# Kernel optimization log

Hardware: AMD Instinct MI355X
Metric: run time of the kernel (lower is better)

## Reference

```python
import jax, jax.numpy as jnp
import numpy as np

L, C, H = 4, 512, 8
HD = C // H

def silu(x):
    return x * jax.nn.sigmoid(x)

def layernorm(x, g, b, eps=1e-5):
    m = x.mean(-1, keepdims=True)
    v = ((x - m) ** 2).mean(-1, keepdims=True)
    return (x - m) * jax.lax.rsqrt(v + eps) * g + b

def adaln(x, t, w, b):
    # x: (N,B,C), t: (B,C), w: (2C,C), b: (2C,)
    mod = silu(t) @ w.T + b
    scale, shift = jnp.split(mod, 2, axis=-1)
    return x * (1.0 + scale[None]) + shift[None]

def embed_rotary(x, pos):
    # x: (B,N,C), pos: (B,N,C,2) with [...,0]=cos, [...,1]=sin
    cos, sin = pos[..., 0], pos[..., 1]
    x2 = jnp.stack([-x[..., 1::2], x[..., 0::2]], axis=-1).reshape(x.shape)
    return x * cos + x2 * sin

def setup_inputs() -> dict:
    key = jax.random.key(0)
    ks = jax.random.split(key, 24)
    Nq, Nkv, B = 1024, 2048, 4
    query = jax.random.normal(ks[0], (Nq, B, C), jnp.float32)
    value = jax.random.normal(ks[1], (Nkv, B, C), jnp.float32)
    diff_ts = jax.random.normal(ks[2], (B, C), jnp.float32)
    # valid rotary codes: cos/sin of random angles
    aq = jax.random.uniform(ks[3], (B, Nq, C), jnp.float32, 0.0, 2 * np.pi)
    ak = jax.random.uniform(ks[4], (B, Nkv, C), jnp.float32, 0.0, 2 * np.pi)
    query_pos = jnp.stack([jnp.cos(aq), jnp.sin(aq)], axis=-1)
    value_pos = jnp.stack([jnp.cos(ak), jnp.sin(ak)], axis=-1)
    s = 0.02
    inp = dict(query=query, value=value, diff_ts=diff_ts,
               query_pos=query_pos, value_pos=value_pos,
               aw_attn=jax.random.normal(ks[5], (L, 2 * C, C)) * s,
               ab_attn=jax.random.normal(ks[6], (L, 2 * C)) * s,
               in_w=jax.random.normal(ks[7], (L, 3 * C, C)) * s,
               in_b=jnp.zeros((L, 3 * C)),
               out_w=jax.random.normal(ks[8], (L, C, C)) * s,
               out_b=jnp.zeros((L, C)),
               ln1_g=jnp.ones((L, C)), ln1_b=jnp.zeros((L, C)),
               aw_ffn=jax.random.normal(ks[9], (L, 2 * C, C)) * s,
               ab_ffn=jax.random.normal(ks[10], (L, 2 * C)) * s,
               w1=jax.random.normal(ks[11], (L, C, C)) * s,
               b1=jnp.zeros((L, C)),
               w2=jax.random.normal(ks[12], (L, C, C)) * s,
               b2=jnp.zeros((L, C)),
               ln2_g=jnp.ones((L, C)), ln2_b=jnp.zeros((L, C)))
    return inp

def _forward(query, value, diff_ts, query_pos, value_pos,
             aw_attn, ab_attn, in_w, in_b, out_w, out_b, ln1_g, ln1_b,
             aw_ffn, ab_ffn, w1, b1, w2, b2, ln2_g, ln2_b):
    Nq, B, _ = query.shape
    Nkv = value.shape[0]
    scaling = HD ** -0.5
    outputs = []
    q = query
    for i in range(L):
        # --- cross-attention layer ---
        aq = adaln(q, diff_ts, aw_attn[i], ab_attn[i])
        wq, wk, wv = jnp.split(in_w[i], 3, axis=0)
        bq, bk, bv = jnp.split(in_b[i], 3, axis=0)
        qp = (aq @ wq.T + bq) * scaling          # (Nq,B,C)
        kp = value @ wk.T + bk                    # (Nkv,B,C)
        vp = value @ wv.T + bv
        qb = embed_rotary(qp.transpose(1, 0, 2), query_pos)  # (B,Nq,C)
        kb = embed_rotary(kp.transpose(1, 0, 2), value_pos)  # (B,Nkv,C)
        vb = vp.transpose(1, 0, 2)
        qh = qb.reshape(B, Nq, H, HD).transpose(0, 2, 1, 3)   # (B,H,Nq,HD)
        kh = kb.reshape(B, Nkv, H, HD).transpose(0, 2, 1, 3)
        vh = vb.reshape(B, Nkv, H, HD).transpose(0, 2, 1, 3)
        scores = jnp.einsum('bhqd,bhkd->bhqk', qh, kh)
        attn = jax.nn.softmax(scores, axis=-1)
        o = jnp.einsum('bhqk,bhkd->bhqd', attn, vh)
        o = o.transpose(0, 2, 1, 3).reshape(B, Nq, C).transpose(1, 0, 2)  # (Nq,B,C)
        o = o @ out_w[i].T + out_b[i]
        q = layernorm(q + o, ln1_g[i], ln1_b[i])
        # --- feedforward layer (residual uses AdaLN-modulated x) ---
        xa = adaln(q, diff_ts, aw_ffn[i], ab_ffn[i])
        h = jax.nn.relu(xa @ w1[i].T + b1[i])
        h = h @ w2[i].T + b2[i]
        q = layernorm(xa + h, ln2_g[i], ln2_b[i])
        outputs.append(q)
    return jnp.stack(outputs)  # (L, Nq, B, C)

def reference(query, value, diff_ts, query_pos, value_pos,
              aw_attn, ab_attn, in_w, in_b, out_w, out_b, ln1_g, ln1_b,
              aw_ffn, ab_ffn, w1, b1, w2, b2, ln2_g, ln2_b):
    return _forward(query, value, diff_ts, query_pos, value_pos,
                    aw_attn, ab_attn, in_w, in_b, out_w, out_b, ln1_g, ln1_b,
                    aw_ffn, ab_ffn, w1, b1, w2, b2, ln2_g, ln2_b)
```

## Files before the change

kernel.cpp:

```cpp
#include <hip/hip_runtime.h>
#include <hip/hip_bf16.h>

typedef __hip_bfloat16 bf16;
typedef __attribute__((ext_vector_type(8))) short short8;
typedef __attribute__((ext_vector_type(4))) short s16x4;
typedef __attribute__((ext_vector_type(4))) float f32x4;

#define CDIM 512
#define BDIM 4
#define HDIM 8
#define HDQ  64
#define NQ   1024
#define NKV  2048
#define LAYERS 4
#define SPLIT 2

#if defined(__has_builtin)
#if __has_builtin(__builtin_amdgcn_global_load_lds)
#define USE_GLL 1
#endif
#endif

static __device__ __forceinline__ short f2s(float f) {
    bf16 h = __float2bfloat16(f);
    return *reinterpret_cast<short*>(&h);
}


__global__ __launch_bounds__(256) void convall_k(
    const float* __restrict__ s0, const float* __restrict__ s1,
    const float* __restrict__ s2, const float* __restrict__ s3,
    const float* __restrict__ s4,
    bf16* __restrict__ d0, bf16* __restrict__ d1, bf16* __restrict__ d2,
    bf16* __restrict__ d3, bf16* __restrict__ d4) {
    int gid = blockIdx.x * 256 + threadIdx.x;
    const float* src; bf16* dst; int off;
    if (gid < 1048576)      { src = s0; dst = d0; off = gid; }
    else if (gid < 1835008) { src = s1; dst = d1; off = gid - 1048576; }
    else if (gid < 2097152) { src = s2; dst = d2; off = gid - 1835008; }
    else if (gid < 2359296) { src = s3; dst = d3; off = gid - 2097152; }
    else                    { src = s4; dst = d4; off = gid - 2359296; }
    f32x4 v = *(const f32x4*)(src + (size_t)off * 4);
    s16x4 o;
    o[0] = f2s(v[0]); o[1] = f2s(v[1]); o[2] = f2s(v[2]); o[3] = f2s(v[3]);
    *(s16x4*)(dst + (size_t)off * 4) = o;
}

__global__ __launch_bounds__(256) void modall_k(const float* __restrict__ diff_ts,
    const float* __restrict__ aw_attn, const float* __restrict__ ab_attn,
    const float* __restrict__ aw_ffn,  const float* __restrict__ ab_ffn,
    float* __restrict__ mod) {
    int wv = blockIdx.x * 4 + (threadIdx.x >> 6);
    int lane = threadIdx.x & 63;
    int col  = wv & 1023;
    int b    = (wv >> 10) & 3;
    int kind = (wv >> 12) & 1;
    int l    = wv >> 13;
    const float* w = (kind ? aw_ffn : aw_attn) + ((size_t)l * 1024 + col) * CDIM + lane * 8;
    const float* tb = diff_ts + b * CDIM + lane * 8;
    f32x4 w0 = *(const f32x4*)w;
    f32x4 w1 = *(const f32x4*)(w + 4);
    f32x4 t0 = *(const f32x4*)tb;
    f32x4 t1 = *(const f32x4*)(tb + 4);
    #pragma unroll
    for (int j = 0; j < 4; ++j) {
        t0[j] = t0[j] / (1.f + __expf(-t0[j]));
        t1[j] = t1[j] / (1.f + __expf(-t1[j]));
    }
    f32x4 pp = w0 * t0 + w1 * t1;
    float acc = (pp[0] + pp[1]) + (pp[2] + pp[3]);
    #pragma unroll
    for (int off = 32; off; off >>= 1) acc += __shfl_xor(acc, off);
    if (lane == 0)
        mod[wv] = acc + (kind ? ab_ffn : ab_attn)[l * 1024 + col];
}

__global__ __launch_bounds__(256) void adaln_k(const float* __restrict__ x,
                                               const float* __restrict__ mod,
                                               bf16* __restrict__ outb) {
    int i = blockIdx.x * 256 + threadIdx.x;
    int c = i & 511;
    int b = (i >> 9) & 3;
    outb[i] = __float2bfloat16(x[i] * (1.f + mod[b * 1024 + c]) + mod[b * 1024 + 512 + c]);
}

__global__ __launch_bounds__(256) void ln_ad_k(const float* __restrict__ x,
                                               const float* __restrict__ res,
                                               const float* __restrict__ g,
                                               const float* __restrict__ bb,
                                               const float* __restrict__ mod,
                                               float* __restrict__ ln_f,
                                               float* __restrict__ ln_f2,
                                               float* __restrict__ ad_f,
                                               bf16* __restrict__ ad_b) {
    int row = blockIdx.x;
    int t = threadIdx.x;
    size_t base = (size_t)row * CDIM;
    float v0 = x[base + t] + res[base + t];
    float v1 = x[base + t + 256] + res[base + t + 256];
    float s1 = v0 + v1;
    float s2 = v0 * v0 + v1 * v1;
    #pragma unroll
    for (int off = 32; off; off >>= 1) {
        s1 += __shfl_xor(s1, off);
        s2 += __shfl_xor(s2, off);
    }
    __shared__ float a1[4], a2[4];
    int w = t >> 6;
    if ((t & 63) == 0) { a1[w] = s1; a2[w] = s2; }
    __syncthreads();
    s1 = a1[0] + a1[1] + a1[2] + a1[3];
    s2 = a2[0] + a2[1] + a2[2] + a2[3];
    float mean = s1 * (1.f / 512.f);
    float var = s2 * (1.f / 512.f) - mean * mean;
    float rs = rsqrtf(var + 1e-5f);
    float y0 = (v0 - mean) * rs * g[t] + bb[t];
    float y1 = (v1 - mean) * rs * g[t + 256] + bb[t + 256];
    if (ln_f)  { ln_f[base + t] = y0;  ln_f[base + t + 256] = y1; }
    if (ln_f2) { ln_f2[base + t] = y0; ln_f2[base + t + 256] = y1; }
    if (mod) {
        int b = row & 3;
        float o0 = y0 * (1.f + mod[b * 1024 + t]) + mod[b * 1024 + 512 + t];
        float o1 = y1 * (1.f + mod[b * 1024 + t + 256]) + mod[b * 1024 + 512 + t + 256];
        if (ad_f) { ad_f[base + t] = o0; ad_f[base + t + 256] = o1; }
        ad_b[base + t] = __float2bfloat16(o0);
        ad_b[base + t + 256] = __float2bfloat16(o1);
    }
}

template <int EPI, int WM, int NT, bool SWZ>
__global__ __launch_bounds__(256) void mgemm_k(
    const bf16* __restrict__ A, const bf16* __restrict__ Wt,
    const float* __restrict__ bias, void* __restrict__ out0v,
    int M, int N, int K,
    const float* __restrict__ pos, float scl, int Nseq) {
    __shared__ bf16 As[2][2][64 * 32];
    __shared__ bf16 Bs[2][2][64 * 32];
    int t = threadIdx.x;
    int w = t >> 6;
    int lane = t & 63;
    int l16 = lane & 15;
    int quad = lane >> 4;
    int wy = w >> 1, wx = w & 1;

    int bxi, byi;
    if (SWZ) {
        int nx = gridDim.x, ny = gridDim.y;
        int flat = blockIdx.y * nx + blockIdx.x;
        int nwg = nx * ny;
        int s = (flat & 7) * (nwg >> 3) + (flat >> 3);
        bxi = s % nx; byi = s / nx;
    } else {
        bxi = blockIdx.x; byi = blockIdx.y;
    }
    int bm = byi * 64;
    int bn = bxi * 64;

    int lr2 = lane >> 2;
    int lc4 = (lane & 3) ^ ((lane >> 3) & 3);

    f32x4 acc[WM][NT] = {};

    auto stage = [&](int buf, int k0) {
#if USE_GLL
        const bf16* sa = A + (size_t)(bm + w * 16 + lr2) * K + k0 + lc4 * 8;
        const bf16* sb = Wt + (size_t)(bn + w * 16 + lr2) * K + k0 + lc4 * 8;
        #pragma unroll
        for (int j = 0; j < 2; ++j) {
            __builtin_amdgcn_global_load_lds(
                (const unsigned int __attribute__((address_space(1)))*)(sa + j * 32),
                (unsigned int __attribute__((address_space(3)))*)(&As[buf][j][w * 512]),
                16, 0, 0);
            __builtin_amdgcn_global_load_lds(
                (const unsigned int __attribute__((address_space(1)))*)(sb + j * 32),
                (unsigned int __attribute__((address_space(3)))*)(&Bs[buf][j][w * 512]),
                16, 0, 0);
        }
#else
        for (int e = t; e < 512; e += 256) {
            int sub = e >> 8, c = e & 255;
            int row = c >> 2, c4 = c & 3;
            int srcc = c4 ^ ((row >> 1) & 3);
            *(uint4*)&As[buf][sub][row * 32 + c4 * 8] =
                *(const uint4*)(A + (size_t)(bm + row) * K + k0 + sub * 32 + srcc * 8);
            *(uint4*)&Bs[buf][sub][row * 32 + c4 * 8] =
                *(const uint4*)(Wt + (size_t)(bn + row) * K + k0 + sub * 32 + srcc * 8);
        }
#endif
    };

    stage(0, 0);
    int cur = 0;
    int rchunk = (quad ^ ((l16 >> 1) & 3)) * 8;

    for (int k0 = 0; k0 < K; k0 += 64) {
        bool more = (k0 + 64 < K);
        if (more) stage(cur ^ 1, k0 + 64);
#if USE_GLL
        if (more) asm volatile("s_waitcnt vmcnt(4)" ::: "memory");
        else      asm volatile("s_waitcnt vmcnt(0)" ::: "memory");
        __builtin_amdgcn_s_barrier();
#else
        __syncthreads();
#endif

        #pragma unroll
        for (int kk = 0; kk < 2; ++kk) {
            short8 af[WM], bfr[NT];
            #pragma unroll
            for (int mt = 0; mt < WM; ++mt)
                af[mt] = *(const short8*)
                    &As[cur][kk][((wy * WM + mt) * 16 + l16) * 32 + rchunk];
            #pragma unroll
            for (int nt = 0; nt < NT; ++nt)
                bfr[nt] = *(const short8*)
                    &Bs[cur][kk][((wx * NT + nt) * 16 + l16) * 32 + rchunk];
            #pragma unroll
            for (int mt = 0; mt < WM; ++mt)
                #pragma unroll
                for (int nt = 0; nt < NT; ++nt)
                    acc[mt][nt] = __builtin_amdgcn_mfma_f32_16x16x32_bf16(
                        af[mt], bfr[nt], acc[mt][nt], 0, 0, 0);
        }

#if USE_GLL
        __builtin_amdgcn_s_barrier();
#else
        __syncthreads();
#endif
        cur ^= 1;
    }

    #pragma unroll
    for (int nt = 0; nt < NT; ++nt) {
        int n = bn + (wx * NT + nt) * 16 + l16;
        float bnv = bias[n];
        #pragma unroll
        for (int mt = 0; mt < WM; ++mt) {
            #pragma unroll
            for (int r = 0; r < 4; ++r) {
                int m = bm + (wy * WM + mt) * 16 + quad * 4 + r;
                float v = acc[mt][nt][r] + bnv;
                if (EPI == 0) {
                    ((float*)out0v)[(size_t)m * N + n] = v;
                } else if (EPI == 1) {
                    ((bf16*)out0v)[(size_t)m * N + n] = __float2bfloat16(fmaxf(v, 0.f));
                } else {
                    v *= scl;
                    int c = n;
                    int nseq = m >> 2, b = m & 3;
                    float part = __shfl_xor(v, 1);
                    const float* pp = pos + (((size_t)b * Nseq + nseq) * CDIM + c) * 2;
                    float cs = pp[0], sn = pp[1];
                    float o = (l16 & 1) ? (v * cs + part * sn) : (v * cs - part * sn);
                    bf16* op = (bf16*)out0v +
                               ((size_t)(b * HDIM + (c >> 6)) * Nseq + nseq) * HDQ + (c & 63);
                    *op = __float2bfloat16(o);
                }
            }
        }
    }
}

__global__ __launch_bounds__(512) void kv8_k(
    const bf16* __restrict__ val, const bf16* __restrict__ Wk,
    const bf16* __restrict__ Wv, const float* __restrict__ biask,
    const float* __restrict__ biasv, bf16* __restrict__ kh,
    bf16* __restrict__ vt, const float* __restrict__ vpos) {
    __shared__ bf16 As[2][2][128 * 32];
    __shared__ bf16 Bk[2][2][64 * 32];
    __shared__ bf16 Bv[2][2][64 * 32];
    int t = threadIdx.x;
    int w = t >> 6;
    int lane = t & 63;
    int l16 = lane & 15;
    int quad = lane >> 4;
    int wy = w >> 1, wx = w & 1;

    int flat = blockIdx.x;
    int s = (flat & 7) * 64 + (flat >> 3);
    int bn = (s & 7) * 64;
    int bm = (s >> 3) * 128;
    const int K = CDIM;

    int lr2 = lane >> 2;
    int lc4 = (lane & 3) ^ ((lane >> 3) & 3);

    f32x4 acck[2][2] = {};
    f32x4 accv[2][2] = {};

    auto stage = [&](int buf, int k0) {
#if USE_GLL
        const bf16* sa = val + (size_t)(bm + w * 16 + lr2) * K + k0 + lc4 * 8;
        #pragma unroll
        for (int j = 0; j < 2; ++j) {
            __builtin_amdgcn_global_load_lds(
                (const unsigned int __attribute__((address_space(1)))*)(sa + j * 32),
                (unsigned int __attribute__((address_space(3)))*)(&As[buf][j][w * 512]),
                16, 0, 0);
        }
        if (w < 4) {
            const bf16* sk = Wk + (size_t)(bn + w * 16 + lr2) * K + k0 + lc4 * 8;
            #pragma unroll
            for (int j = 0; j < 2; ++j) {
                __builtin_amdgcn_global_load_lds(
                    (const unsigned int __attribute__((address_space(1)))*)(sk + j * 32),
                    (unsigned int __attribute__((address_space(3)))*)(&Bk[buf][j][w * 512]),
                    16, 0, 0);
            }
        } else {
            const bf16* sv = Wv + (size_t)(bn + (w - 4) * 16 + lr2) * K + k0 + lc4 * 8;
            #pragma unroll
            for (int j = 0; j < 2; ++j) {
                __builtin_amdgcn_global_load_lds(
                    (const unsigned int __attribute__((address_space(1)))*)(sv + j * 32),
                    (unsigned int __attribute__((address_space(3)))*)(&Bv[buf][j][(w - 4) * 512]),
                    16, 0, 0);
            }
        }
#else
        for (int u = t; u < 1024; u += 512) {
            int sub = u >> 9, c = u & 511;
            int row = c >> 2, c4 = c & 3;
            int srcc = c4 ^ ((row >> 1) & 3);
            *(uint4*)&As[buf][sub][row * 32 + c4 * 8] =
                *(const uint4*)(val + (size_t)(bm + row) * K + k0 + sub * 32 + srcc * 8);
        }
        {
            int u = t;
            int sub = u >> 8, c = u & 255;
            int row = c >> 2, c4 = c & 3;
            int srcc = c4 ^ ((row >> 1) & 3);
            *(uint4*)&Bk[buf][sub][row * 32 + c4 * 8] =
                *(const uint4*)(Wk + (size_t)(bn + row) * K + k0 + sub * 32 + srcc * 8);
            *(uint4*)&Bv[buf][sub][row * 32 + c4 * 8] =
                *(const uint4*)(Wv + (size_t)(bn + row) * K + k0 + sub * 32 + srcc * 8);
        }
#endif
    };

    stage(0, 0);
    int cur = 0;
    int rchunk = (quad ^ ((l16 >> 1) & 3)) * 8;

    for (int k0 = 0; k0 < K; k0 += 64) {
        bool more = (k0 + 64 < K);
        if (more) stage(cur ^ 1, k0 + 64);
#if USE_GLL
        if (more) asm volatile("s_waitcnt vmcnt(4)" ::: "memory");
        else      asm volatile("s_waitcnt vmcnt(0)" ::: "memory");
        __builtin_amdgcn_s_barrier();
#else
        __syncthreads();
#endif

        #pragma unroll
        for (int kk = 0; kk < 2; ++kk) {
            short8 af[2], bkf[2], bvf[2];
            #pragma unroll
            for (int mt = 0; mt < 2; ++mt)
                af[mt] = *(const short8*)
                    &As[cur][kk][(wy * 32 + mt * 16 + l16) * 32 + rchunk];
            #pragma unroll
            for (int nt = 0; nt < 2; ++nt) {
                bkf[nt] = *(const short8*)
                    &Bk[cur][kk][((wx * 2 + nt) * 16 + l16) * 32 + rchunk];
                bvf[nt] = *(const short8*)
                    &Bv[cur][kk][((wx * 2 + nt) * 16 + l16) * 32 + rchunk];
            }
            #pragma unroll
            for (int mt = 0; mt < 2; ++mt)
                #pragma unroll
                for (int nt = 0; nt < 2; ++nt) {
                    acck[mt][nt] = __builtin_amdgcn_mfma_f32_16x16x32_bf16(
                        af[mt], bkf[nt], acck[mt][nt], 0, 0, 0);
                    accv[mt][nt] = __builtin_amdgcn_mfma_f32_16x16x32_bf16(
                        af[mt], bvf[nt], accv[mt][nt], 0, 0, 0);
                }
        }

#if USE_GLL
        __builtin_amdgcn_s_barrier();
#else
        __syncthreads();
#endif
        cur ^= 1;
    }

    #pragma unroll
    for (int nt = 0; nt < 2; ++nt) {
        int n = bn + (wx * 2 + nt) * 16 + l16;
        float bk_n = biask[n];
        float bv_n = biasv[n];
        int d = n & 63, hh = n >> 6;
        #pragma unroll
        for (int mt = 0; mt < 2; ++mt) {
            #pragma unroll
            for (int r = 0; r < 4; ++r) {
                int m = bm + wy * 32 + mt * 16 + quad * 4 + r;
                int nseq = m >> 2, b = m & 3;
                float v = acck[mt][nt][r] + bk_n;
                float part = __shfl_xor(v, 1);
                const float* pp = vpos + (((size_t)b * NKV + nseq) * CDIM + n) * 2;
                float cs = pp[0], sn = pp[1];
                float o = (l16 & 1) ? (v * cs + part * sn) : (v * cs - part * sn);
                kh[((size_t)(b * HDIM + hh) * NKV + nseq) * HDQ + d] =
                    __float2bfloat16(o);
                float vv = accv[mt][nt][r] + bv_n;
                vt[((size_t)(b * HDIM + hh) * HDQ + d) * NKV + nseq] =
                    __float2bfloat16(vv);
            }
        }
    }
}

__global__ __launch_bounds__(512) void attn8_k(const bf16* __restrict__ qh,
                                               const bf16* __restrict__ kh,
                                               const bf16* __restrict__ vT,
                                               float* __restrict__ pl,
                                               float* __restrict__ pacc) {
    __shared__ short Kb[2][64 * 64];
    __shared__ short Vb[2][64 * 64];
    __shared__ short Ps[8][16 * 64];
    int t = threadIdx.x;
    int wave = t >> 6, lane = t & 63;
    int l16 = lane & 15, quad = lane >> 4;

    int b0 = blockIdx.x;
    int newid = (b0 & 7) * 64 + (b0 >> 3);
    int qtile = newid & 7;
    int grp = newid >> 3;
    int split = grp & 1;
    int bh = grp >> 1;
    int q0 = qtile * 128 + wave * 16;
    int kbase = split * (NKV / SPLIT);

    const bf16* qbase = qh + ((size_t)bh * NQ + q0) * HDQ;
    short8 aq0 = *(const short8*)(qbase + (size_t)l16 * HDQ + quad * 8);
    short8 aq1 = *(const short8*)(qbase + (size_t)l16 * HDQ + 32 + quad * 8);
    const bf16* kbh = kh + ((size_t)bh * NKV + kbase) * HDQ;
    const bf16* vbh = vT + (size_t)bh * HDQ * NKV + kbase;

    int r0 = wave * 8;
    int lr = lane >> 3;
    int swz_src = ((lane & 7) ^ lr) * 8;

    auto stage = [&](int buf, int kt) {
#if USE_GLL
        __builtin_amdgcn_global_load_lds(
            (const unsigned int __attribute__((address_space(1)))*)
                (kbh + (size_t)(kt + r0 + lr) * HDQ + swz_src),
            (unsigned int __attribute__((address_space(3)))*)&Kb[buf][r0 * 64],
            16, 0, 0);
        __builtin_amdgcn_global_load_lds(
            (const unsigned int __attribute__((address_space(1)))*)
                (vbh + (size_t)(r0 + lr) * NKV + kt + swz_src),
            (unsigned int __attribute__((address_space(3)))*)&Vb[buf][r0 * 64],
            16, 0, 0);
#else
        int rr = r0 + lr;
        int lc = lane & 7;
        *(short8*)&Kb[buf][rr * 64 + ((lc ^ (rr & 7)) * 8)] =
            *(const short8*)(kbh + (size_t)(kt + rr) * HDQ + lc * 8);
        *(short8*)&Vb[buf][rr * 64 + ((lc ^ (rr & 7)) * 8)] =
            *(const short8*)(vbh + (size_t)rr * NKV + kt + lc * 8);
#endif
    };

    f32x4 accO[4] = {};
    float lsum[4] = {0.f, 0.f, 0.f, 0.f};

    stage(0, 0);
    int cur = 0;
    int swz_m = l16 & 7;

    for (int kt = 0; kt < NKV / SPLIT; kt += 64) {
        bool more = (kt + 64 < NKV / SPLIT);
        if (more) stage(cur ^ 1, kt + 64);
#if USE_GLL
        if (more) asm volatile("s_waitcnt vmcnt(2)" ::: "memory");
        else      asm volatile("s_waitcnt vmcnt(0)" ::: "memory");
        __builtin_amdgcn_s_barrier();
#else
        __syncthreads();
#endif

        f32x4 sc[4] = {};
        #pragma unroll
        for (int nt = 0; nt < 4; ++nt) {
            const short* kr = &Kb[cur][(nt * 16 + l16) * 64];
            short8 bk0 = *(const short8*)&kr[(quad ^ swz_m) * 8];
            short8 bk1 = *(const short8*)&kr[((quad + 4) ^ swz_m) * 8];
            sc[nt] = __builtin_amdgcn_mfma_f32_16x16x32_bf16(aq0, bk0, sc[nt], 0, 0, 0);
            sc[nt] = __builtin_amdgcn_mfma_f32_16x16x32_bf16(aq1, bk1, sc[nt], 0, 0, 0);
        }

        #pragma unroll
        for (int r = 0; r < 4; ++r) {
            float p0 = exp2f(sc[0][r]);
            float p1 = exp2f(sc[1][r]);
            float p2 = exp2f(sc[2][r]);
            float p3 = exp2f(sc[3][r]);
            lsum[r] += (p0 + p1) + (p2 + p3);
            int pr = quad * 4 + r;
            short* prow = &Ps[wave][pr * 64];
            int pm = pr & 7;
            int ch = l16 >> 3, kl = l16 & 7;
            prow[((ch ^ pm) << 3) + kl]       = f2s(p0);
            prow[(((ch + 2) ^ pm) << 3) + kl] = f2s(p1);
            prow[(((ch + 4) ^ pm) << 3) + kl] = f2s(p2);
            prow[(((ch + 6) ^ pm) << 3) + kl] = f2s(p3);
        }

        const short* prd = &Ps[wave][l16 * 64];
        short8 pa0 = *(const short8*)&prd[(quad ^ swz_m) * 8];
        short8 pa1 = *(const short8*)&prd[((quad + 4) ^ swz_m) * 8];
        #pragma unroll
        for (int nt = 0; nt < 4; ++nt) {
            const short* vr = &Vb[cur][(nt * 16 + l16) * 64];
            short8 bv0 = *(const short8*)&vr[(quad ^ swz_m) * 8];
            short8 bv1 = *(const short8*)&vr[((quad + 4) ^ swz_m) * 8];
            accO[nt] = __builtin_amdgcn_mfma_f32_16x16x32_bf16(pa0, bv0, accO[nt], 0, 0, 0);
            accO[nt] = __builtin_amdgcn_mfma_f32_16x16x32_bf16(pa1, bv1, accO[nt], 0, 0, 0);
        }

#if USE_GLL
        __builtin_amdgcn_s_barrier();
#else
        __syncthreads();
#endif
        cur ^= 1;
    }

    #pragma unroll
    for (int r = 0; r < 4; ++r) {
        #pragma unroll
        for (int off = 1; off < 16; off <<= 1) lsum[r] += __shfl_xor(lsum[r], off);
    }

    size_t rowbase = ((size_t)split * 32 + bh) * NQ + q0;
    #pragma unroll
    for (int r = 0; r < 4; ++r) {
        size_t row = rowbase + quad * 4 + r;
        if (l16 == 0) pl[row] = lsum[r];
        #pragma unroll
        for (int nt = 0; nt < 4; ++nt)
            pacc[row * 64 + nt * 16 + l16] = accO[nt][r];
    }
}

__global__ __launch_bounds__(256) void attn_comb_k(const float* __restrict__ pl,
                                                   const float* __restrict__ pacc,
                                                   bf16* __restrict__ o) {
    int idx = blockIdx.x * 256 + threadIdx.x;
    int d4 = (idx & 15) << 2;
    int row = idx >> 4;
    int q = row & (NQ - 1);
    int bh = row >> 10;
    const int S = 32 * NQ;
    float rl = 1.0f / (pl[row] + pl[S + row]);
    f32x4 a = *(const f32x4*)&pacc[(size_t)row * 64 + d4];
    f32x4 b = *(const f32x4*)&pacc[(size_t)(S + row) * 64 + d4];
    int bsel = bh >> 3, h = bh & 7;
    s16x4 o4;
    #pragma unroll
    for (int j = 0; j < 4; ++j) o4[j] = f2s((a[j] + b[j]) * rl);
    *(s16x4*)&o[((size_t)(q * BDIM + bsel)) * CDIM + h * HDQ + d4] = o4;
}


extern "C" void kernel_launch(void* const* d_in, const int* in_sizes, int n_in,
                              void* d_out, int out_size, void* d_ws, size_t ws_size,
                              hipStream_t stream) {
    const float* query     = (const float*)d_in[0];
    const float* value     = (const float*)d_in[1];
    const float* diff_ts   = (const float*)d_in[2];
    const float* query_pos = (const float*)d_in[3];
    const float* value_pos = (const float*)d_in[4];
    const float* aw_attn   = (const float*)d_in[5];
    const float* ab_attn   = (const float*)d_in[6];
    const float* in_w      = (const float*)d_in[7];
    const float* in_b      = (const float*)d_in[8];
    const float* out_w     = (const float*)d_in[9];
    const float* out_b     = (const float*)d_in[10];
    const float* ln1_g     = (const float*)d_in[11];
    const float* ln1_b     = (const float*)d_in[12];
    const float* aw_ffn    = (const float*)d_in[13];
    const float* ab_ffn    = (const float*)d_in[14];
    const float* w1        = (const float*)d_in[15];
    const float* b1        = (const float*)d_in[16];
    const float* w2        = (const float*)d_in[17];
    const float* b2        = (const float*)d_in[18];
    const float* ln2_g     = (const float*)d_in[19];
    const float* ln2_b     = (const float*)d_in[20];
    float* out_f = (float*)d_out;

    float* ws      = (float*)d_ws;
    float* mod_ws  = ws + 2048;
    float* q_cur   = ws + 34816;
    float* buf_a   = q_cur + 2097152;
    float* buf_p   = buf_a + 2097152;
    bf16* a_bf     = (bf16*)(buf_p + 2097152);
    bf16* h_bf     = a_bf + 2097152;
    bf16* qh       = h_bf + 2097152;
    bf16* kh       = qh + 2097152;
    bf16* vt       = kh + 4194304;
    bf16* val_bf   = vt + 4194304;
    bf16* winb     = val_bf + 4194304;
    bf16* woutb    = winb + 3145728;
    bf16* w1b      = woutb + 1048576;
    bf16* w2b      = w1b + 1048576;
    float* pacc    = buf_a;
    float* pl      = (float*)a_bf;

    const int MQ = NQ * BDIM;
    const float scaling = 0.125f * 1.44269504f;

    modall_k<<<8192, 256, 0, stream>>>(diff_ts, aw_attn, ab_attn, aw_ffn, ab_ffn, mod_ws);
    convall_k<<<10240, 256, 0, stream>>>(value, in_w, out_w, w1, w2,
                                         val_bf, winb, woutb, w1b, w2b);
    adaln_k<<<(MQ * CDIM) / 256, 256, 0, stream>>>(query, mod_ws, a_bf);

    for (int i = 0; i < LAYERS; ++i) {
        const float* mod_ffn  = mod_ws + i * 8192 + 4096;
        const float* mod_attn_next = (i + 1 < LAYERS) ? (mod_ws + (i + 1) * 8192) : nullptr;
        const bf16* winb_i = winb + (size_t)i * 1536 * CDIM;
        const float* in_b_i = in_b + (size_t)i * 1536;
        const float* qsrc = (i == 0) ? query : q_cur;

        mgemm_k<2, 2, 2, true><<<dim3(8, MQ / 64), 256, 0, stream>>>(
            a_bf, winb_i, in_b_i, qh, MQ, 512, CDIM, query_pos, scaling, NQ);
        kv8_k<<<512, 512, 0, stream>>>(
            val_bf, winb_i + (size_t)512 * CDIM, winb_i + (size_t)1024 * CDIM,
            in_b_i + 512, in_b_i + 1024, kh, vt, value_pos);
        attn8_k<<<512, 512, 0, stream>>>(qh, kh, vt, pl, pacc);
        attn_comb_k<<<2048, 256, 0, stream>>>(pl, pacc, h_bf);
        mgemm_k<0, 2, 2, true><<<dim3(8, MQ / 64), 256, 0, stream>>>(
            h_bf, woutb + (size_t)i * CDIM * CDIM, out_b + i * CDIM, buf_p,
            MQ, 512, CDIM, nullptr, 0.f, 0);
        ln_ad_k<<<MQ, 256, 0, stream>>>(qsrc, buf_p,
                                        ln1_g + i * CDIM, ln1_b + i * CDIM,
                                        mod_ffn, nullptr, nullptr, buf_a, a_bf);
        mgemm_k<1, 2, 2, true><<<dim3(8, MQ / 64), 256, 0, stream>>>(
            a_bf, w1b + (size_t)i * CDIM * CDIM, b1 + i * CDIM, h_bf,
            MQ, 512, CDIM, nullptr, 0.f, 0);
        mgemm_k<0, 2, 2, true><<<dim3(8, MQ / 64), 256, 0, stream>>>(
            h_bf, w2b + (size_t)i * CDIM * CDIM, b2 + i * CDIM, buf_p,
            MQ, 512, CDIM, nullptr, 0.f, 0);
        ln_ad_k<<<MQ, 256, 0, stream>>>(buf_a, buf_p,
                                        ln2_g + i * CDIM, ln2_b + i * CDIM,
                                        mod_attn_next, q_cur,
                                        out_f + (size_t)i * MQ * CDIM, nullptr, a_bf);
    }
}
```

Before: 659.6 us.

## Fuse Q projection into K/V projection kernel as extra blocks

Merges the separate Q-projection GEMM (with rotary epilogue) and the K/V projection kernel into one launch of 768 blocks, where blocks 512+ compute Q using the same 128x64 tiling and only the first weight buffer. This removes one kernel launch per layer and lets Q and KV work overlap on the GPU. The Q path now uses a 512-thread tile shape instead of the previous mgemm configuration, and it has wave-dependent vmcnt waits because waves 4-7 issue fewer loads.

Result: faster. 633.2 us (-4.0%).

```diff
diff --git a/kernel.cpp b/kernel.cpp
--- a/kernel.cpp
+++ b/kernel.cpp
@@ -243,55 +243,52 @@
                 float v = acc[mt][nt][r] + bnv;
                 if (EPI == 0) {
                     ((float*)out0v)[(size_t)m * N + n] = v;
-                } else if (EPI == 1) {
+                } else {
                     ((bf16*)out0v)[(size_t)m * N + n] = __float2bfloat16(fmaxf(v, 0.f));
-                } else {
-                    v *= scl;
-                    int c = n;
-                    int nseq = m >> 2, b = m & 3;
-                    float part = __shfl_xor(v, 1);
-                    const float* pp = pos + (((size_t)b * Nseq + nseq) * CDIM + c) * 2;
-                    float cs = pp[0], sn = pp[1];
-                    float o = (l16 & 1) ? (v * cs + part * sn) : (v * cs - part * sn);
-                    bf16* op = (bf16*)out0v +
-                               ((size_t)(b * HDIM + (c >> 6)) * Nseq + nseq) * HDQ + (c & 63);
-                    *op = __float2bfloat16(o);
                 }
             }
         }
     }
 }
 
-__global__ __launch_bounds__(512) void kv8_k(
-    const bf16* __restrict__ val, const bf16* __restrict__ Wk,
-    const bf16* __restrict__ Wv, const float* __restrict__ biask,
-    const float* __restrict__ biasv, bf16* __restrict__ kh,
-    bf16* __restrict__ vt, const float* __restrict__ vpos) {
+__global__ __launch_bounds__(512) void qkv8_k(
+    const bf16* __restrict__ a_bf, const bf16* __restrict__ val,
+    const bf16* __restrict__ winb_i, const float* __restrict__ in_b_i,
+    bf16* __restrict__ qh, bf16* __restrict__ kh, bf16* __restrict__ vt,
+    const float* __restrict__ qpos, const float* __restrict__ vpos,
+    float scaling) {
     __shared__ bf16 As[2][2][128 * 32];
-    __shared__ bf16 Bk[2][2][64 * 32];
-    __shared__ bf16 Bv[2][2][64 * 32];
+    __shared__ bf16 B0[2][2][64 * 32];
+    __shared__ bf16 B1[2][2][64 * 32];
     int t = threadIdx.x;
     int w = t >> 6;
     int lane = t & 63;
     int l16 = lane & 15;
     int quad = lane >> 4;
     int wy = w >> 1, wx = w & 1;
-
-    int flat = blockIdx.x;
-    int s = (flat & 7) * 64 + (flat >> 3);
-    int bn = (s & 7) * 64;
-    int bm = (s >> 3) * 128;
     const int K = CDIM;
+
+    bool isq = (blockIdx.x >= 512);
+    int bm, bn;
+    const bf16 *Aptr, *W0, *W1;
+    if (isq) {
+        int flat = blockIdx.x - 512;
+        int s = (flat & 7) * 32 + (flat >> 3);
+        bn = (s & 7) * 64; bm = (s >> 3) * 128;
+        Aptr = a_bf; W0 = winb_i; W1 = nullptr;
+    } else {
+        int flat = blockIdx.x;
+        int s = (flat & 7) * 64 + (flat >> 3);
+        bn = (s & 7) * 64; bm = (s >> 3) * 128;
+        Aptr = val; W0 = winb_i + (size_t)512 * CDIM; W1 = winb_i + (size_t)1024 * CDIM;
+    }
 
     int lr2 = lane >> 2;
     int lc4 = (lane & 3) ^ ((lane >> 3) & 3);
 
-    f32x4 acck[2][2] = {};
-    f32x4 accv[2][2] = {};
-
     auto stage = [&](int buf, int k0) {
 #if USE_GLL
-        const bf16* sa = val + (size_t)(bm + w * 16 + lr2) * K + k0 + lc4 * 8;
+        const bf16* sa = Aptr + (size_t)(bm + w * 16 + lr2) * K + k0 + lc4 * 8;
         #pragma unroll
         for (int j = 0; j < 2; ++j) {
             __builtin_amdgcn_global_load_lds(
@@ -300,21 +297,21 @@
                 16, 0, 0);
         }
         if (w < 4) {
-            const bf16* sk = Wk + (size_t)(bn + w * 16 + lr2) * K + k0 + lc4 * 8;
+            const bf16* sk = W0 + (size_t)(bn + w * 16 + lr2) * K + k0 + lc4 * 8;
             #pragma unroll
             for (int j = 0; j < 2; ++j) {
                 __builtin_amdgcn_global_load_lds(
                     (const unsigned int __attribute__((address_space(1)))*)(sk + j * 32),
-                    (unsigned int __attribute__((address_space(3)))*)(&Bk[buf][j][w * 512]),
+                    (unsigned int __attribute__((address_space(3)))*)(&B0[buf][j][w * 512]),
                     16, 0, 0);
             }
-        } else {
-            const bf16* sv = Wv + (size_t)(bn + (w - 4) * 16 + lr2) * K + k0 + lc4 * 8;
+        } else if (!isq) {
+            const bf16* sv = W1 + (size_t)(bn + (w - 4) * 16 + lr2) * K + k0 + lc4 * 8;
             #pragma unroll
             for (int j = 0; j < 2; ++j) {
                 __builtin_amdgcn_global_load_lds(
                     (const unsigned int __attribute__((address_space(1)))*)(sv + j * 32),
-                    (unsigned int __attribute__((address_space(3)))*)(&Bv[buf][j][(w - 4) * 512]),
+                    (unsigned int __attribute__((address_space(3)))*)(&B1[buf][j][(w - 4) * 512]),
                     16, 0, 0);
             }
         }
@@ -324,91 +321,156 @@
             int row = c >> 2, c4 = c & 3;
             int srcc = c4 ^ ((row >> 1) & 3);
             *(uint4*)&As[buf][sub][row * 32 + c4 * 8] =
-                *(const uint4*)(val + (size_t)(bm + row) * K + k0 + sub * 32 + srcc * 8);
+                *(const uint4*)(Aptr + (size_t)(bm + row) * K + k0 + sub * 32 + srcc * 8);
         }
         {
             int u = t;
             int sub = u >> 8, c = u & 255;
             int row = c >> 2, c4 = c & 3;
             int srcc = c4 ^ ((row >> 1) & 3);
-            *(uint4*)&Bk[buf][sub][row * 32 + c4 * 8] =
-                *(const uint4*)(Wk + (size_t)(bn + row) * K + k0 + sub * 32 + srcc * 8);
-            *(uint4*)&Bv[buf][sub][row * 32 + c4 * 8] =
-                *(const uint4*)(Wv + (size_t)(bn + row) * K + k0 + sub * 32 + srcc * 8);
+            *(uint4*)&B0[buf][sub][row * 32 + c4 * 8] =
+                *(const uint4*)(W0 + (size_t)(bn + row) * K + k0 + sub * 32 + srcc * 8);
+            if (!isq)
+                *(uint4*)&B1[buf][sub][row * 32 + c4 * 8] =
+                    *(const uint4*)(W1 + (size_t)(bn + row) * K + k0 + sub * 32 + srcc * 8);
         }
 #endif
     };
 
+    int rchunk = (quad ^ ((l16 >> 1) & 3)) * 8;
     stage(0, 0);
     int cur = 0;
-    int rchunk = (quad ^ ((l16 >> 1) & 3)) * 8;
-
-    for (int k0 = 0; k0 < K; k0 += 64) {
-        bool more = (k0 + 64 < K);
-        if (more) stage(cur ^ 1, k0 + 64);
-#if USE_GLL
-        if (more) asm volatile("s_waitcnt vmcnt(4)" ::: "memory");
-        else      asm volatile("s_waitcnt vmcnt(0)" ::: "memory");
-        __builtin_amdgcn_s_barrier();
-#else
-        __syncthreads();
-#endif
-
-        #pragma unroll
-        for (int kk = 0; kk < 2; ++kk) {
-            short8 af[2], bkf[2], bvf[2];
-            #pragma unroll
-            for (int mt = 0; mt < 2; ++mt)
-                af[mt] = *(const short8*)
-                    &As[cur][kk][(wy * 32 + mt * 16 + l16) * 32 + rchunk];
-            #pragma unroll
-            for (int nt = 0; nt < 2; ++nt) {
-                bkf[nt] = *(const short8*)
-                    &Bk[cur][kk][((wx * 2 + nt) * 16 + l16) * 32 + rchunk];
-                bvf[nt] = *(const short8*)
-                    &Bv[cur][kk][((wx * 2 + nt) * 16 + l16) * 32 + rchunk];
+
+    if (isq) {
+        f32x4 acc[2][2] = {};
+        for (int k0 = 0; k0 < K; k0 += 64) {
+            bool more = (k0 + 64 < K);
+            if (more) stage(cur ^ 1, k0 + 64);
+#if USE_GLL
+            if (more) {
+                if (w < 4) asm volatile("s_waitcnt vmcnt(4)" ::: "memory");
+                else       asm volatile("s_waitcnt vmcnt(2)" ::: "memory");
+            } else {
+                asm volatile("s_waitcnt vmcnt(0)" ::: "memory");
             }
-            #pragma unroll
-            for (int mt = 0; mt < 2; ++mt)
+            __builtin_amdgcn_s_barrier();
+#else
+            __syncthreads();
+#endif
+            #pragma unroll
+            for (int kk = 0; kk < 2; ++kk) {
+                short8 af[2], bfr[2];
+                #pragma unroll
+                for (int mt = 0; mt < 2; ++mt)
+                    af[mt] = *(const short8*)
+                        &As[cur][kk][(wy * 32 + mt * 16 + l16) * 32 + rchunk];
+                #pragma unroll
+                for (int nt = 0; nt < 2; ++nt)
+                    bfr[nt] = *(const short8*)
+                        &B0[cur][kk][((wx * 2 + nt) * 16 + l16) * 32 + rchunk];
+                #pragma unroll
+                for (int mt = 0; mt < 2; ++mt)
+                    #pragma unroll
+                    for (int nt = 0; nt < 2; ++nt)
+                        acc[mt][nt] = __builtin_amdgcn_mfma_f32_16x16x32_bf16(
+                            af[mt], bfr[nt], acc[mt][nt], 0, 0, 0);
+            }
+#if USE_GLL
+            __builtin_amdgcn_s_barrier();
+#else
+            __syncthreads();
+#endif
+            cur ^= 1;
+        }
+
+        #pragma unroll
+        for (int nt = 0; nt < 2; ++nt) {
+            int n = bn + (wx * 2 + nt) * 16 + l16;
+            float bnv = in_b_i[n];
+            #pragma unroll
+            for (int mt = 0; mt < 2; ++mt) {
+                #pragma unroll
+                for (int r = 0; r < 4; ++r) {
+                    int m = bm + wy * 32 + mt * 16 + quad * 4 + r;
+                    float v = (acc[mt][nt][r] + bnv) * scaling;
+                    int nseq = m >> 2, b = m & 3;
+                    float part = __shfl_xor(v, 1);
+                    const float* pp = qpos + (((size_t)b * NQ + nseq) * CDIM + n) * 2;
+                    float cs = pp[0], sn = pp[1];
+                    float o = (l16 & 1) ? (v * cs + part * sn) : (v * cs - part * sn);
+                    qh[((size_t)(b * HDIM + (n >> 6)) * NQ + nseq) * HDQ + (n & 63)] =
+                        __float2bfloat16(o);
+                }
+            }
+        }
+    } else {
+        f32x4 acck[2][2] = {};
+        f32x4 accv[2][2] = {};
+        for (int k0 = 0; k0 < K; k0 += 64) {
+            bool more = (k0 + 64 < K);
+            if (more) stage(cur ^ 1, k0 + 64);
+#if USE_GLL
+            if (more) asm volatile("s_waitcnt vmcnt(4)" ::: "memory");
+            else      asm volatile("s_waitcnt vmcnt(0)" ::: "memory");
+            __builtin_amdgcn_s_barrier();
+#else
+            __syncthreads();
+#endif
+            #pragma unroll
+            for (int kk = 0; kk < 2; ++kk) {
+                short8 af[2], bkf[2], bvf[2];
+                #pragma unroll
+                for (int mt = 0; mt < 2; ++mt)
+                    af[mt] = *(const short8*)
+                        &As[cur][kk][(wy * 32 + mt * 16 + l16) * 32 + rchunk];
                 #pragma unroll
                 for (int nt = 0; nt < 2; ++nt) {
-                    acck[mt][nt] = __builtin_amdgcn_mfma_f32_16x16x32_bf16(
-                        af[mt], bkf[nt], acck[mt][nt], 0, 0, 0);
-                    accv[mt][nt] = __builtin_amdgcn_mfma_f32_16x16x32_bf16(
-                        af[mt], bvf[nt], accv[mt][nt], 0, 0, 0);
+                    bkf[nt] = *(const short8*)
+                        &B0[cur][kk][((wx * 2 + nt) * 16 + l16) * 32 + rchunk];
+                    bvf[nt] = *(const short8*)
+                        &B1[cur][kk][((wx * 2 + nt) * 16 + l16) * 32 + rchunk];
                 }
-        }
-
-#if USE_GLL
-        __builtin_amdgcn_s_barrier();
-#else
-        __syncthreads();
-#endif
-        cur ^= 1;
-    }
-
-    #pragma unroll
-    for (int nt = 0; nt < 2; ++nt) {
-        int n = bn + (wx * 2 + nt) * 16 + l16;
-        float bk_n = biask[n];
-        float bv_n = biasv[n];
-        int d = n & 63, hh = n >> 6;
-        #pragma unroll
-        for (int mt = 0; mt < 2; ++mt) {
-            #pragma unroll
-            for (int r = 0; r < 4; ++r) {
-                int m = bm + wy * 32 + mt * 16 + quad * 4 + r;
-                int nseq = m >> 2, b = m & 3;
-                float v = acck[mt][nt][r] + bk_n;
-                float part = __shfl_xor(v, 1);
-                const float* pp = vpos + (((size_t)b * NKV + nseq) * CDIM + n) * 2;
-                float cs = pp[0], sn = pp[1];
-                float o = (l16 & 1) ? (v * cs + part * sn) : (v * cs - part * sn);
-                kh[((size_t)(b * HDIM + hh) * NKV + nseq) * HDQ + d] =
-                    __float2bfloat16(o);
-                float vv = accv[mt][nt][r] + bv_n;
-                vt[((size_t)(b * HDIM + hh) * HDQ + d) * NKV + nseq] =
-                    __float2bfloat16(vv);
+                #pragma unroll
+                for (int mt = 0; mt < 2; ++mt)
+                    #pragma unroll
+                    for (int nt = 0; nt < 2; ++nt) {
+                        acck[mt][nt] = __builtin_amdgcn_mfma_f32_16x16x32_bf16(
+                            af[mt], bkf[nt], acck[mt][nt], 0, 0, 0);
+                        accv[mt][nt] = __builtin_amdgcn_mfma_f32_16x16x32_bf16(
+                            af[mt], bvf[nt], accv[mt][nt], 0, 0, 0);
+                    }
+            }
+#if USE_GLL
+            __builtin_amdgcn_s_barrier();
+#else
+            __syncthreads();
+#endif
+            cur ^= 1;
+        }
+
+        #pragma unroll
+        for (int nt = 0; nt < 2; ++nt) {
+            int n = bn + (wx * 2 + nt) * 16 + l16;
+            float bk_n = in_b_i[512 + n];
+            float bv_n = in_b_i[1024 + n];
+            int d = n & 63, hh = n >> 6;
+            #pragma unroll
+            for (int mt = 0; mt < 2; ++mt) {
+                #pragma unroll
+                for (int r = 0; r < 4; ++r) {
+                    int m = bm + wy * 32 + mt * 16 + quad * 4 + r;
+                    int nseq = m >> 2, b = m & 3;
+                    float v = acck[mt][nt][r] + bk_n;
+                    float part = __shfl_xor(v, 1);
+                    const float* pp = vpos + (((size_t)b * NKV + nseq) * CDIM + n) * 2;
+                    float cs = pp[0], sn = pp[1];
+                    float o = (l16 & 1) ? (v * cs + part * sn) : (v * cs - part * sn);
+                    kh[((size_t)(b * HDIM + hh) * NKV + nseq) * HDQ + d] =
+                        __float2bfloat16(o);
+                    float vv = accv[mt][nt][r] + bv_n;
+                    vt[((size_t)(b * HDIM + hh) * HDQ + d) * NKV + nseq] =
+                        __float2bfloat16(vv);
+                }
             }
         }
     }
@@ -628,11 +690,8 @@
         const float* in_b_i = in_b + (size_t)i * 1536;
         const float* qsrc = (i == 0) ? query : q_cur;
 
-        mgemm_k<2, 2, 2, true><<<dim3(8, MQ / 64), 256, 0, stream>>>(
-            a_bf, winb_i, in_b_i, qh, MQ, 512, CDIM, query_pos, scaling, NQ);
-        kv8_k<<<512, 512, 0, stream>>>(
-            val_bf, winb_i + (size_t)512 * CDIM, winb_i + (size_t)1024 * CDIM,
-            in_b_i + 512, in_b_i + 1024, kh, vt, value_pos);
+        qkv8_k<<<768, 512, 0, stream>>>(a_bf, val_bf, winb_i, in_b_i,
+                                        qh, kh, vt, query_pos, value_pos, scaling);
         attn8_k<<<512, 512, 0, stream>>>(qh, kh, vt, pl, pacc);
         attn_comb_k<<<2048, 256, 0, stream>>>(pl, pacc, h_bf);
         mgemm_k<0, 2, 2, true><<<dim3(8, MQ / 64), 256, 0, stream>>>(
```
